# Performance work log

Measured on AMD Instinct MI355X. Metric: run time of the kernel, lower is better.

The kernel has to match this reference:

```python
import jax, jax.numpy as jnp
import numpy as np

# ---- static hyperparams (from comp_encoding.__init__ / DMPNNEncoderLayer) ----
B = 512            # number of molecules in the batch (wrapper's python loop)
A = 128            # padded atoms per molecule == max_mol_len
E = 256            # padded directed bonds per molecule
K = 6              # max incoming bonds gathered per bond/atom
ATOM_FDIM = 133
BOND_FDIM = 14
H = 128            # d_hidden = max_mol_len
DEPTH = 3
G = 2048           # global feature dim (Morgan fingerprint)


def _mol_lens():
    ml = np.array(jax.random.randint(jax.random.fold_in(jax.random.key(0), 5), (B,), 16, H + 1))
    ml[0] = H  # ensure comp_dim == max(mol_lens) == H so per-row padding is a no-op
    return ml


def setup_inputs() -> dict:
    key = jax.random.key(0)
    ks = jax.random.split(key, 10)
    atom_feature = jax.random.normal(ks[0], (B, A, ATOM_FDIM), jnp.float32)
    f_ini_atoms_bond = jax.random.normal(ks[1], (B, E, ATOM_FDIM + BOND_FDIM), jnp.float32)
    atom_to_incoming_bond = jax.random.randint(ks[2], (B, A, K), 0, E)
    mapping = jax.random.randint(ks[3], (B, E, K), 0, E)
    global_f = jax.random.normal(ks[4], (B, G), jnp.float32)
    mol_lens = _mol_lens()  # static numpy ints (constants, drive output shapes)
    W_i = jax.random.normal(ks[6], (H, ATOM_FDIM + BOND_FDIM), jnp.float32) / np.float32(np.sqrt(ATOM_FDIM + BOND_FDIM))
    W_h = jax.random.normal(ks[7], (H, H), jnp.float32) / np.float32(np.sqrt(H))
    W_o = jax.random.normal(ks[8], (H, ATOM_FDIM + H), jnp.float32) / np.float32(np.sqrt(ATOM_FDIM + H))
    b_o = jax.random.normal(ks[9], (H,), jnp.float32) * 0.01
    return dict(atom_feature=atom_feature, f_ini_atoms_bond=f_ini_atoms_bond,
                atom_to_incoming_bond=atom_to_incoming_bond, mapping=mapping,
                global_f=global_f, mol_lens=mol_lens,
                W_i=W_i, W_h=W_h, W_o=W_o, b_o=b_o)


def _gather_sum(msg, idx):
    # msg: [B, E, H]; idx: [B, N, K] -> sum over K incoming messages: [B, N, H]
    b, n, k = idx.shape
    g = jnp.take_along_axis(msg, idx.reshape(b, n * k)[..., None], axis=1)
    return g.reshape(b, n, k, -1).sum(axis=2)


def reference(atom_feature, f_ini_atoms_bond, atom_to_incoming_bond, mapping,
              global_f, mol_lens, W_i, W_h, W_o, b_o):
    # DMPNN: W_i on initial directed-bond features
    inp = jnp.einsum('bef,hf->beh', f_ini_atoms_bond, W_i)   # [B, E, H]
    msg = jax.nn.relu(inp)
    for _ in range(DEPTH - 1):
        agg = _gather_sum(msg, mapping)                      # [B, E, H]
        msg = jax.nn.relu(inp + jnp.einsum('beh,gh->beg', agg, W_h))
    m2a = _gather_sum(msg, atom_to_incoming_bond)            # [B, A, H]
    cat = jnp.concatenate([atom_feature, m2a], axis=-1)      # [B, A, 133+H]
    atoms_h = jax.nn.relu(jnp.einsum('bad,hd->bah', cat, W_o) + b_o)  # [B, A, H]

    # wrapper: take first mol_len atom encodings per molecule, stack, build mask
    ml = np.asarray(mol_lens)
    valid = np.arange(A)[None, :] < ml[:, None]              # [B, A] static
    b_idx, a_idx = np.nonzero(valid)
    comp = atoms_h[b_idx, a_idx]                             # [sum(mol_lens), H]
    c_mask = jnp.asarray(valid.astype(np.float32))           # [B, comp_dim]
    return comp, c_mask
```

## Files before the change

### kernel.cpp

```cpp
#include <hip/hip_runtime.h>
#include <hip/hip_bf16.h>

typedef unsigned int   uint;
typedef unsigned short ushort;
typedef short bf16x8 __attribute__((ext_vector_type(8)));
typedef float f32x4  __attribute__((ext_vector_type(4)));

constexpr int Bm   = 512;
constexpr int Aa   = 128;
constexpr int Ee   = 256;
constexpr int Kk   = 6;
constexpr int AFD  = 133;
constexpr int FD   = 147;
constexpr int Hh   = 128;
constexpr int CATD = 261;
constexpr int KWI  = 192;
constexpr int KWO  = 320;
constexpr int MST  = 136;
constexpr int APAD = 832;

__device__ __forceinline__ ushort f2b(float f) {
    uint u = __float_as_uint(f);
    u += 0x7FFFu + ((u >> 16) & 1u);
    return (ushort)(u >> 16);
}
__device__ __forceinline__ uint cvt2(float x, float y) {
    float2 t2; t2.x = x; t2.y = y;
    __hip_bfloat162 t = __float22bfloat162_rn(t2);
    uint r; __builtin_memcpy(&r, &t, 4); return r;
}
__device__ __forceinline__ float2 b2f2(uint p) {
    float2 r;
    r.x = __uint_as_float(p << 16);
    r.y = __uint_as_float(p & 0xFFFF0000u);
    return r;
}

__device__ __forceinline__ bf16x8 gsum6(const ushort* src, const int* mr, int ko) {
    float2 s0 = {0.f, 0.f}, s1 = {0.f, 0.f}, s2 = {0.f, 0.f}, s3 = {0.f, 0.f};
#pragma unroll
    for (int k = 0; k < Kk; ++k) {
        uint4 m = *(const uint4*)&src[mr[k] + ko];
        float2 a = b2f2(m.x); s0.x += a.x; s0.y += a.y;
        float2 b = b2f2(m.y); s1.x += b.x; s1.y += b.y;
        float2 d = b2f2(m.z); s2.x += d.x; s2.y += d.y;
        float2 e = b2f2(m.w); s3.x += e.x; s3.y += e.y;
    }
    uint4 o;
    o.x = cvt2(s0.x, s0.y); o.y = cvt2(s1.x, s1.y);
    o.z = cvt2(s2.x, s2.y); o.w = cvt2(s3.x, s3.y);
    bf16x8 r;
    __builtin_memcpy(&r, &o, 16);
    return r;
}

__device__ __forceinline__ bf16x8 ld_frag_f32(const float* sp, int c0, int lim) {
    float v[8];
#pragma unroll
    for (int d = 0; d < 8; ++d) v[d] = (c0 + d < lim) ? sp[d] : 0.f;
    uint4 o;
    o.x = cvt2(v[0], v[1]); o.y = cvt2(v[2], v[3]);
    o.z = cvt2(v[4], v[5]); o.w = cvt2(v[6], v[7]);
    bf16x8 r;
    __builtin_memcpy(&r, &o, 16);
    return r;
}

__global__ __launch_bounds__(256) void k_prep_w(const float* __restrict__ Wi,
                                                const float* __restrict__ Wh,
                                                const float* __restrict__ Wo,
                                                ushort* __restrict__ Wi_b,
                                                ushort* __restrict__ Wh_b,
                                                ushort* __restrict__ Wo_b) {
    const int h = blockIdx.x, t = threadIdx.x;
    for (int c = t; c < KWI; c += 256)
        Wi_b[h * KWI + c] = f2b(c < FD ? Wi[h * FD + c] : 0.f);
    for (int c = t; c < Hh; c += 256)
        Wh_b[h * Hh + c] = f2b(Wh[h * Hh + c]);
    for (int c = t; c < KWO; c += 256) {
        float v = 0.f;
        if (c < AFD)       v = Wo[h * CATD + c];
        else if (c >= 192) v = Wo[h * CATD + AFD + (c - 192)];
        Wo_b[h * KWO + c] = f2b(v);
    }
}

__global__ __launch_bounds__(512) void k_scan(const int* __restrict__ ml,
                                              int* __restrict__ pfx) {
    __shared__ int s[512];
    int t = threadIdx.x;
    s[t] = ml[t];
    __syncthreads();
    for (int off = 1; off < 512; off <<= 1) {
        int v = (t >= off) ? s[t - off] : 0;
        __syncthreads();
        s[t] += v;
        __syncthreads();
    }
    pfx[t + 1] = s[t];
    if (t == 0) pfx[0] = 0;
}

__global__ __launch_bounds__(1024, 1) void k_fused(
        const float* __restrict__ atomf,
        const float* __restrict__ fini,
        const int*   __restrict__ a2ib,
        const int*   __restrict__ mapping,
        const ushort* __restrict__ Wi_b,
        const ushort* __restrict__ Wh_b,
        const ushort* __restrict__ Wo_b,
        const float* __restrict__ bo,
        const int*   __restrict__ mol_lens,
        const int*   __restrict__ pfx,
        float* __restrict__ out,
        float* __restrict__ cmask) {
    __shared__ ushort msg[Ee * MST];
    __shared__ int    map_s[Ee * Kk];
    __shared__ int    a2_s[Aa * Kk + APAD];

    const int b    = blockIdx.x;
    const int tid  = threadIdx.x;
    const int wave = tid >> 6;
    const int lane = tid & 63;
    const int l15  = lane & 15, quad = lane >> 4;

    for (int i = tid; i < Ee * Kk; i += 1024) map_s[i] = mapping[b * Ee * Kk + i];
    for (int i = tid; i < Aa * Kk; i += 1024) a2_s[i]  = a2ib[b * Aa * Kk + i];
    const int len = mol_lens[b];
    if (tid < Aa) cmask[b * Aa + tid] = (tid < len) ? 1.0f : 0.0f;

    const int brow = wave * 16 + l15;

    f32x4 acc[8];
#pragma unroll
    for (int j = 0; j < 8; ++j) acc[j] = (f32x4){0.f, 0.f, 0.f, 0.f};

    const float* fsrc = fini + (size_t)b * Ee * FD;
#pragma unroll
    for (int c = 0; c < 3; ++c) {
#pragma unroll
        for (int ks = 0; ks < 2; ++ks) {
            const int c0 = c * 64 + ks * 32 + quad * 8;
            bf16x8 af = ld_frag_f32(fsrc + (size_t)brow * FD + c0, c0, FD);
#pragma unroll
            for (int jh = 0; jh < 2; ++jh) {
                bf16x8 bf[4];
#pragma unroll
                for (int j = 0; j < 4; ++j)
                    bf[j] = *(const bf16x8*)&Wi_b[((jh * 4 + j) * 16 + l15) * KWI + c0];
#pragma unroll
                for (int j = 0; j < 4; ++j)
                    acc[jh * 4 + j] = __builtin_amdgcn_mfma_f32_16x16x32_bf16(
                        af, bf[j], acc[jh * 4 + j], 0, 0, 0);
            }
        }
    }

    uint2 inp_pk[8];
#pragma unroll
    for (int j = 0; j < 8; ++j) {
        f32x4 a4 = acc[j];
        uint2 p;
        p.x = cvt2(a4[0], a4[1]);
        p.y = cvt2(a4[2], a4[3]);
        inp_pk[j] = p;
        int col = j * 16 + l15;
#pragma unroll
        for (int reg = 0; reg < 4; ++reg) {
            int row = wave * 16 + quad * 4 + reg;
            float v = a4[reg] > 0.f ? a4[reg] : 0.f;
            msg[row * MST + col] = f2b(v);
        }
    }
    __syncthreads();

    int mr[Kk];
#pragma unroll
    for (int k = 0; k < Kk; ++k) mr[k] = map_s[brow * Kk + k] * MST;

#pragma unroll
    for (int h = 0; h < 2; ++h) {
#pragma unroll
        for (int j = 0; j < 8; ++j) {
            float2 lo = b2f2(inp_pk[j].x);
            float2 hi = b2f2(inp_pk[j].y);
            acc[j] = (f32x4){lo.x, lo.y, hi.x, hi.y};
        }
#pragma unroll
        for (int ks = 0; ks < 4; ++ks) {
            const int ko = ks * 32 + quad * 8;
            bf16x8 af = gsum6(msg, mr, ko);
#pragma unroll
            for (int jh = 0; jh < 2; ++jh) {
                bf16x8 bf[4];
#pragma unroll
                for (int j = 0; j < 4; ++j)
                    bf[j] = *(const bf16x8*)&Wh_b[((jh * 4 + j) * 16 + l15) * Hh + ko];
#pragma unroll
                for (int j = 0; j < 4; ++j)
                    acc[jh * 4 + j] = __builtin_amdgcn_mfma_f32_16x16x32_bf16(
                        af, bf[j], acc[jh * 4 + j], 0, 0, 0);
            }
        }
        __syncthreads();
#pragma unroll
        for (int j = 0; j < 8; ++j) {
            int col = j * 16 + l15;
#pragma unroll
            for (int reg = 0; reg < 4; ++reg) {
                int row = wave * 16 + quad * 4 + reg;
                float v = acc[j][reg];
                msg[row * MST + col] = f2b(v > 0.f ? v : 0.f);
            }
        }
        __syncthreads();
    }

    f32x4 ro[4];
#pragma unroll
    for (int j = 0; j < 4; ++j) ro[j] = (f32x4){0.f, 0.f, 0.f, 0.f};

    const int arow = (wave >> 1) * 16 + l15;
    const int ch   = (wave & 1) * 64;

    {
        int ar[Kk];
#pragma unroll
        for (int k = 0; k < Kk; ++k) ar[k] = a2_s[arow * Kk + k] * MST;
#pragma unroll
        for (int ks = 0; ks < 4; ++ks) {
            const int ko = ks * 32 + quad * 8;
            bf16x8 a0 = gsum6(msg, ar, ko);
            bf16x8 bf[4];
#pragma unroll
            for (int j = 0; j < 4; ++j)
                bf[j] = *(const bf16x8*)&Wo_b[(ch + j * 16 + l15) * KWO + 192 + ko];
#pragma unroll
            for (int j = 0; j < 4; ++j)
                ro[j] = __builtin_amdgcn_mfma_f32_16x16x32_bf16(
                    a0, bf[j], ro[j], 0, 0, 0);
        }
    }

    const float* asrc = atomf + (size_t)b * Aa * AFD;
#pragma unroll
    for (int c = 0; c < 3; ++c) {
#pragma unroll
        for (int ks = 0; ks < 2; ++ks) {
            const int c0 = c * 64 + ks * 32 + quad * 8;
            bf16x8 a0 = ld_frag_f32(asrc + (size_t)arow * AFD + c0, c0, AFD);
            bf16x8 bf[4];
#pragma unroll
            for (int j = 0; j < 4; ++j)
                bf[j] = *(const bf16x8*)&Wo_b[(ch + j * 16 + l15) * KWO + c0];
#pragma unroll
            for (int j = 0; j < 4; ++j)
                ro[j] = __builtin_amdgcn_mfma_f32_16x16x32_bf16(
                    a0, bf[j], ro[j], 0, 0, 0);
        }
    }

    const int base = pfx[b];
#pragma unroll
    for (int j = 0; j < 4; ++j) {
        int col = ch + j * 16 + l15;
        float bv = bo[col];
#pragma unroll
        for (int reg = 0; reg < 4; ++reg) {
            int a = (wave >> 1) * 16 + quad * 4 + reg;
            if (a < len) {
                float v = ro[j][reg] + bv;
                out[(size_t)(base + a) * Hh + col] = v > 0.f ? v : 0.f;
            }
        }
    }
}

extern "C" void kernel_launch(void* const* d_in, const int* in_sizes, int n_in,
                              void* d_out, int out_size, void* d_ws, size_t ws_size,
                              hipStream_t stream) {
    const float* atom_feature = (const float*)d_in[0];
    const float* f_ini        = (const float*)d_in[1];
    const int*   a2ib         = (const int*)d_in[2];
    const int*   mapping      = (const int*)d_in[3];
    const int*   mol_lens     = (const int*)d_in[5];
    const float* Wi           = (const float*)d_in[6];
    const float* Wh           = (const float*)d_in[7];
    const float* Wo           = (const float*)d_in[8];
    const float* bo           = (const float*)d_in[9];
    float* out = (float*)d_out;

    ushort* Wi_b = (ushort*)d_ws;
    ushort* Wh_b = Wi_b + 128 * KWI;
    ushort* Wo_b = Wh_b + 128 * Hh;
    int*    pfx  = (int*)(Wo_b + 128 * KWO);

    float* cmask = out + ((size_t)out_size - (size_t)Bm * Aa);

    k_prep_w<<<128, 256, 0, stream>>>(Wi, Wh, Wo, Wi_b, Wh_b, Wo_b);
    k_scan  <<<1, 512, 0, stream>>>(mol_lens, pfx);
    k_fused <<<Bm, 1024, 0, stream>>>(atom_feature, f_ini, a2ib, mapping,
                                      Wi_b, Wh_b, Wo_b, bo, mol_lens, pfx,
                                      out, cmask);
}
```

Measured before the change: 311.9 us.

## Recompute W_i input projection per depth step instead of holding it in registers

Stops keeping the packed bf16 input projection in registers across message-passing steps. Each depth iteration now re-reads the fp32 bond features from global memory and redoes the W_i MFMA as the accumulator's starting value, which lowers register pressure. The K loop over bond features is trimmed from 6 to 5 chunks of 32, which still covers the 147 feature columns. The LDS padding on the atom-index array is removed. The cost is two extra global feature reads and projection GEMMs per molecule.

Result: slower. 429.6 us (+37.7%).

```diff
diff --git a/kernel.cpp b/kernel.cpp
--- a/kernel.cpp
+++ b/kernel.cpp
@@ -17,7 +17,6 @@
 constexpr int KWI  = 192;
 constexpr int KWO  = 320;
 constexpr int MST  = 136;
-constexpr int APAD = 832;
 
 __device__ __forceinline__ ushort f2b(float f) {
     uint u = __float_as_uint(f);
@@ -116,7 +115,7 @@
         float* __restrict__ cmask) {
     __shared__ ushort msg[Ee * MST];
     __shared__ int    map_s[Ee * Kk];
-    __shared__ int    a2_s[Aa * Kk + APAD];
+    __shared__ int    a2_s[Aa * Kk];
 
     const int b    = blockIdx.x;
     const int tid  = threadIdx.x;
@@ -130,17 +129,51 @@
     if (tid < Aa) cmask[b * Aa + tid] = (tid < len) ? 1.0f : 0.0f;
 
     const int brow = wave * 16 + l15;
+    const float* fsrc = fini + (size_t)b * Ee * FD;
 
     f32x4 acc[8];
+
 #pragma unroll
     for (int j = 0; j < 8; ++j) acc[j] = (f32x4){0.f, 0.f, 0.f, 0.f};
-
-    const float* fsrc = fini + (size_t)b * Ee * FD;
-#pragma unroll
-    for (int c = 0; c < 3; ++c) {
-#pragma unroll
-        for (int ks = 0; ks < 2; ++ks) {
-            const int c0 = c * 64 + ks * 32 + quad * 8;
+#pragma unroll
+    for (int ks = 0; ks < 5; ++ks) {
+        const int c0 = ks * 32 + quad * 8;
+        bf16x8 af = ld_frag_f32(fsrc + (size_t)brow * FD + c0, c0, FD);
+#pragma unroll
+        for (int jh = 0; jh < 2; ++jh) {
+            bf16x8 bf[4];
+#pragma unroll
+            for (int j = 0; j < 4; ++j)
+                bf[j] = *(const bf16x8*)&Wi_b[((jh * 4 + j) * 16 + l15) * KWI + c0];
+#pragma unroll
+            for (int j = 0; j < 4; ++j)
+                acc[jh * 4 + j] = __builtin_amdgcn_mfma_f32_16x16x32_bf16(
+                    af, bf[j], acc[jh * 4 + j], 0, 0, 0);
+        }
+    }
+#pragma unroll
+    for (int j = 0; j < 8; ++j) {
+        const int col = j * 16 + l15;
+#pragma unroll
+        for (int reg = 0; reg < 4; ++reg) {
+            const int row = wave * 16 + quad * 4 + reg;
+            float v = acc[j][reg];
+            msg[row * MST + col] = f2b(v > 0.f ? v : 0.f);
+        }
+    }
+    __syncthreads();
+
+#pragma unroll
+    for (int h = 0; h < 2; ++h) {
+        int mr[Kk];
+#pragma unroll
+        for (int k = 0; k < Kk; ++k) mr[k] = map_s[brow * Kk + k] * MST;
+#pragma unroll
+        for (int j = 0; j < 8; ++j) acc[j] = (f32x4){0.f, 0.f, 0.f, 0.f};
+
+#pragma unroll
+        for (int ks = 0; ks < 5; ++ks) {
+            const int c0 = ks * 32 + quad * 8;
             bf16x8 af = ld_frag_f32(fsrc + (size_t)brow * FD + c0, c0, FD);
 #pragma unroll
             for (int jh = 0; jh < 2; ++jh) {
@@ -154,38 +187,6 @@
                         af, bf[j], acc[jh * 4 + j], 0, 0, 0);
             }
         }
-    }
-
-    uint2 inp_pk[8];
-#pragma unroll
-    for (int j = 0; j < 8; ++j) {
-        f32x4 a4 = acc[j];
-        uint2 p;
-        p.x = cvt2(a4[0], a4[1]);
-        p.y = cvt2(a4[2], a4[3]);
-        inp_pk[j] = p;
-        int col = j * 16 + l15;
-#pragma unroll
-        for (int reg = 0; reg < 4; ++reg) {
-            int row = wave * 16 + quad * 4 + reg;
-            float v = a4[reg] > 0.f ? a4[reg] : 0.f;
-            msg[row * MST + col] = f2b(v);
-        }
-    }
-    __syncthreads();
-
-    int mr[Kk];
-#pragma unroll
-    for (int k = 0; k < Kk; ++k) mr[k] = map_s[brow * Kk + k] * MST;
-
-#pragma unroll
-    for (int h = 0; h < 2; ++h) {
-#pragma unroll
-        for (int j = 0; j < 8; ++j) {
-            float2 lo = b2f2(inp_pk[j].x);
-            float2 hi = b2f2(inp_pk[j].y);
-            acc[j] = (f32x4){lo.x, lo.y, hi.x, hi.y};
-        }
 #pragma unroll
         for (int ks = 0; ks < 4; ++ks) {
             const int ko = ks * 32 + quad * 8;
@@ -205,10 +206,10 @@
         __syncthreads();
 #pragma unroll
         for (int j = 0; j < 8; ++j) {
-            int col = j * 16 + l15;
+            const int col = j * 16 + l15;
 #pragma unroll
             for (int reg = 0; reg < 4; ++reg) {
-                int row = wave * 16 + quad * 4 + reg;
+                const int row = wave * 16 + quad * 4 + reg;
                 float v = acc[j][reg];
                 msg[row * MST + col] = f2b(v > 0.f ? v : 0.f);
             }
@@ -263,11 +264,11 @@
     const int base = pfx[b];
 #pragma unroll
     for (int j = 0; j < 4; ++j) {
-        int col = ch + j * 16 + l15;
-        float bv = bo[col];
+        const int col = ch + j * 16 + l15;
+        const float bv = bo[col];
 #pragma unroll
         for (int reg = 0; reg < 4; ++reg) {
-            int a = (wave >> 1) * 16 + quad * 4 + reg;
+            const int a = (wave >> 1) * 16 + quad * 4 + reg;
             if (a < len) {
                 float v = ro[j][reg] + bv;
                 out[(size_t)(base + a) * Hh + col] = v > 0.f ? v : 0.f;
```
